# Kernel tuning notes

Measured on AMD Instinct MI355X. Metric: run time of the kernel, lower is better.

The kernel has to match this reference:

```python
import jax, jax.numpy as jnp
import numpy as np

EPSILON = 1e-05


def setup_inputs() -> dict:
    key = jax.random.key(0)
    k1, k2, k3 = jax.random.split(key, 3)
    B, T, D, K = 8, 4096, 256, 2048
    hidden_states = jax.random.normal(k1, (B, T, D), dtype=jnp.float32)
    embed_sum = jax.random.normal(k2, (K, D), dtype=jnp.float32)
    # cluster usage counts are positive in practice
    cluster_usage = jax.random.uniform(k3, (K,), dtype=jnp.float32) * 10.0 + 0.1
    return {
        "hidden_states": hidden_states,
        "embed_sum": embed_sum,
        "cluster_usage": cluster_usage,
    }


def reference(hidden_states, embed_sum, cluster_usage):
    # embed = embed_sum / clamp(cluster_usage, eps)   -> [K, D]
    embed = embed_sum / jnp.clip(cluster_usage, EPSILON, None)[:, None]

    shape = hidden_states.shape
    x = hidden_states.reshape(-1, shape[-1])  # [N, D]

    # squared L2 distances via norm expansion (argmin equals argmin of cdist p=2)
    x_sq = jnp.sum(x * x, axis=-1, keepdims=True)          # [N, 1]
    e_sq = jnp.sum(embed * embed, axis=-1)[None, :]         # [1, K]
    dots = jnp.einsum("nd,kd->nk", x, embed)               # [N, K]
    dists = x_sq - 2.0 * dots + e_sq                        # [N, K]

    embed_ind = jnp.argmin(dists, axis=-1)                 # [N]
    embed_ind = embed_ind.reshape(shape[:-1])              # [B, T]

    # decode: embedding lookup
    quantize = embed[embed_ind]                             # [B, T, D]
    return quantize, embed_ind
```

## Files before the change

### kernel.cpp

```cpp
#include <hip/hip_runtime.h>
#include <float.h>
#include <stdint.h>


#define EPSILON 1e-5f
#define DELTA   1e-3f

constexpr int D     = 256;
constexpr int K_TOT = 2048;

constexpr int RES_H      = 32768;
constexpr int ESQ_H      = 65536;
constexpr int LDS_HALVES = 69632;
constexpr int DYN_LDS    = LDS_HALVES * 2;

typedef _Float16 half8v __attribute__((ext_vector_type(8)));
typedef _Float16 half4v __attribute__((ext_vector_type(4)));
typedef float    f32x4  __attribute__((ext_vector_type(4)));

#define GLL(SRC, DST)                                                   \
  __builtin_amdgcn_global_load_lds(                                     \
      (const __attribute__((address_space(1))) void*)(SRC),             \
      (__attribute__((address_space(3))) void*)(DST), 16, 0, 0)

__global__ void prep_kernel(const float* __restrict__ es,
                            const float* __restrict__ usage,
                            _Float16* __restrict__ ec,
                            float* __restrict__ esq,
                            int* __restrict__ counter) {
  const int bx   = blockIdx.x;
  const int t    = threadIdx.x;
  const int wid  = t >> 6;
  const int lane = t & 63;
  if (bx < K_TOT / 4) {
    const int k = bx * 4 + wid;
    const float u = fmaxf(usage[k], EPSILON);
    const float4 v = *(const float4*)(es + (size_t)k * D + lane * 4);
    float4 e;
    e.x = v.x / u; e.y = v.y / u; e.z = v.z / u; e.w = v.w / u;
    half4v h, lo;
    h.x = (_Float16)e.x; lo.x = (_Float16)(e.x - (float)h.x);
    h.y = (_Float16)e.y; lo.y = (_Float16)(e.y - (float)h.y);
    h.z = (_Float16)e.z; lo.z = (_Float16)(e.z - (float)h.z);
    h.w = (_Float16)e.w; lo.w = (_Float16)(e.w - (float)h.w);
    *(half4v*)(ec + (size_t)k * 512 + lane * 4)       = h;
    *(half4v*)(ec + (size_t)k * 512 + 256 + lane * 4) = lo;
    float s = e.x * e.x + e.y * e.y + e.z * e.z + e.w * e.w;
    #pragma unroll
    for (int m = 1; m < 64; m <<= 1) s += __shfl_xor(s, m, 64);
    if (lane == 0) esq[k] = s;
  } else {
    if (t == 0) *counter = 0;
  }
}

__global__ __launch_bounds__(512, 2)
void mm_kernel(const float* __restrict__ x, const _Float16* __restrict__ ec,
               const float* __restrict__ esq, const float* __restrict__ es,
               const float* __restrict__ usage,
               float* __restrict__ out_q, float* __restrict__ out_i,
               int* __restrict__ list, int* __restrict__ counter,
               unsigned long long* __restrict__ rmin, int N) {
  extern __shared__ __align__(16) _Float16 lds[];
  const int t    = threadIdx.x;
  const int lane = t & 63;
  const int q    = lane >> 4;
  const int l15  = lane & 15;
  const int wid  = t >> 6;
  const int wn   = wid >> 1;
  const int wk   = wid & 1;
  const int n0   = blockIdx.x * 128;

  float* esq_lds = (float*)&lds[ESQ_H];
  {
    const float4 ev = *(const float4*)(esq + t * 4);
    *(float4*)&esq_lds[t * 4] = ev;
  }

  const int prow  = t >> 2;
  const int pc    = t & 3;
  const int wbase = (t >> 6) * 512 + ((t & 63) ^ ((t >> 3) & 3)) * 8;
  #pragma unroll
  for (int i = 0; i < 8; ++i) {
    const float* src = x + (size_t)(n0 + prow) * D + i * 32 + pc * 8;
    const float4 f0 = *(const float4*)src;
    const float4 f1 = *(const float4*)(src + 4);
    const float f[8] = {f0.x, f0.y, f0.z, f0.w, f1.x, f1.y, f1.z, f1.w};
    half8v hv, lv;
    #pragma unroll
    for (int e = 0; e < 8; ++e) {
      const _Float16 h = (_Float16)f[e];
      hv[e] = h;
      lv[e] = (_Float16)(f[e] - (float)h);
    }
    *(half8v*)&lds[i * 4096 + wbase]         = hv;
    *(half8v*)&lds[RES_H + i * 4096 + wbase] = lv;
  }
  __syncthreads();

  const int gA = l15 * 4 + q;
  const int sp = (gA ^ ((l15 >> 1) & 3)) * 8;

  half8v ahr[8][2];
  #pragma unroll
  for (int s = 0; s < 8; ++s)
    #pragma unroll
    for (int mi = 0; mi < 2; ++mi)
      ahr[s][mi] = *(const half8v*)&lds[s * 4096 + wn * 1024 + mi * 512 + sp];
  __syncthreads();

  const int r0 = t >> 3;
  const int cl = (t & 7) ^ (r0 & 7);
  const _Float16* pB = ec + (size_t)r0 * 512 + cl * 8;

  #pragma unroll
  for (int s = 0; s < 3; ++s) {
    const _Float16* sp0 = pB + s * 64;
    GLL(sp0,         &lds[s * 8192 + t * 8]);
    GLL(sp0 + 32768, &lds[s * 8192 + 4096 + t * 8]);
  }

  int bfoff[4][2];
  #pragma unroll
  for (int ni = 0; ni < 4; ++ni)
    #pragma unroll
    for (int j = 0; j < 2; ++j)
      bfoff[ni][j] = (wk * 64 + ni * 16 + l15) * 64 +
                     (((j << 2) + q) ^ (l15 & 7)) * 8;

  float rd0[2][4], rd1[2][4];
  int   ri0[2][4];
  #pragma unroll
  for (int mi = 0; mi < 2; ++mi)
    #pragma unroll
    for (int r = 0; r < 4; ++r) {
      rd0[mi][r] = FLT_MAX; rd1[mi][r] = FLT_MAX; ri0[mi][r] = 0x7fffffff;
    }

  for (int kt = 0; kt < 16; ++kt) {
    int   kc[4];
    float eqv[4];
    #pragma unroll
    for (int ni = 0; ni < 4; ++ni) {
      kc[ni]  = kt * 128 + wk * 64 + ni * 16 + l15;
      eqv[ni] = esq_lds[kc[ni]];
    }

    f32x4 acc[2][4] = {};

    #pragma unroll
    for (int sidx = 0; sidx < 8; ++sidx) {
      const int ss = kt * 8 + sidx;
      if (kt == 15 && sidx == 6)
        asm volatile("s_waitcnt vmcnt(2)" ::: "memory");
      else if (kt == 15 && sidx == 7)
        asm volatile("s_waitcnt vmcnt(0)" ::: "memory");
      else
        asm volatile("s_waitcnt vmcnt(4)" ::: "memory");
      __builtin_amdgcn_s_barrier();
      __builtin_amdgcn_sched_barrier(0);

      if (!(kt == 15 && sidx >= 5)) {
        const int ns = ss + 3;
        const _Float16* np = pB + (size_t)(ns >> 3) * 65536 + (ns & 7) * 64;
        const int nb = (ns & 3) * 8192;
        GLL(np,         &lds[nb + t * 8]);
        GLL(np + 32768, &lds[nb + 4096 + t * 8]);
      }

      const int bb = (ss & 3) * 8192;
      __builtin_amdgcn_s_setprio(1);
      #pragma unroll
      for (int j = 0; j < 2; ++j) {
        half8v bf[4];
        #pragma unroll
        for (int ni = 0; ni < 4; ++ni)
          bf[ni] = *(const half8v*)&lds[bb + bfoff[ni][j]];
        const int ks = (sidx & 3) * 2 + j;
        if (sidx < 4) {
          half8v al[2];
          #pragma unroll
          for (int mi = 0; mi < 2; ++mi)
            al[mi] = *(const half8v*)
                &lds[RES_H + ks * 4096 + wn * 1024 + mi * 512 + sp];
          #pragma unroll
          for (int mi = 0; mi < 2; ++mi)
            #pragma unroll
            for (int ni = 0; ni < 4; ++ni)
              acc[mi][ni] = __builtin_amdgcn_mfma_f32_16x16x32_f16(
                  ahr[ks][mi], bf[ni], acc[mi][ni], 0, 0, 0);
          #pragma unroll
          for (int mi = 0; mi < 2; ++mi)
            #pragma unroll
            for (int ni = 0; ni < 4; ++ni)
              acc[mi][ni] = __builtin_amdgcn_mfma_f32_16x16x32_f16(
                  al[mi], bf[ni], acc[mi][ni], 0, 0, 0);
        } else {
          #pragma unroll
          for (int mi = 0; mi < 2; ++mi)
            #pragma unroll
            for (int ni = 0; ni < 4; ++ni)
              acc[mi][ni] = __builtin_amdgcn_mfma_f32_16x16x32_f16(
                  ahr[ks][mi], bf[ni], acc[mi][ni], 0, 0, 0);
        }
      }
      __builtin_amdgcn_s_setprio(0);
    }

    #pragma unroll
    for (int ni = 0; ni < 4; ++ni) {
      #pragma unroll
      for (int mi = 0; mi < 2; ++mi) {
        #pragma unroll
        for (int r = 0; r < 4; ++r) {
          const float d = fmaf(-2.f, acc[mi][ni][r], eqv[ni]);
          if (d < rd0[mi][r]) {
            rd1[mi][r] = rd0[mi][r]; rd0[mi][r] = d; ri0[mi][r] = kc[ni];
          } else {
            rd1[mi][r] = fminf(rd1[mi][r], d);
          }
        }
      }
    }
  }
  __syncthreads();

  float* ex = (float*)lds;
  #pragma unroll
  for (int mi = 0; mi < 2; ++mi) {
    #pragma unroll
    for (int r = 0; r < 4; ++r) {
      float d0 = rd0[mi][r], d1 = rd1[mi][r];
      int   i0 = ri0[mi][r];
      #pragma unroll
      for (int off = 1; off < 16; off <<= 1) {
        const float od0 = __shfl_xor(d0, off, 16);
        const int   oi0 = __shfl_xor(i0, off, 16);
        const float od1 = __shfl_xor(d1, off, 16);
        if (od0 < d0 || (od0 == d0 && oi0 < i0)) {
          d1 = fminf(d0, od1); d0 = od0; i0 = oi0;
        } else {
          d1 = fminf(d1, od0);
        }
      }
      if (l15 == mi * 8 + r) {
        const int row = wn * 32 + mi * 16 + q * 4 + r;
        *(float4*)&ex[(row * 2 + wk) * 4] =
            make_float4(d0, __int_as_float(i0), d1, 0.f);
      }
    }
  }
  __syncthreads();

  {
    const int row = t >> 2;
    const int seg = t & 3;
    const float4 a = *(const float4*)&ex[(row * 2 + 0) * 4];
    const float4 b = *(const float4*)&ex[(row * 2 + 1) * 4];
    float d0, d1; int i0;
    const int ia = __float_as_int(a.y), ib = __float_as_int(b.y);
    if (b.x < a.x || (b.x == a.x && ib < ia)) {
      d0 = b.x; i0 = ib; d1 = fminf(a.x, b.z);
    } else {
      d0 = a.x; i0 = ia; d1 = fminf(a.z, b.x);
    }
    const int n = n0 + row;
    const float u  = fmaxf(usage[i0], EPSILON);
    const float4* src = (const float4*)(es + (size_t)i0 * D);
    float4*       dst = (float4*)(out_q + (size_t)n * D);
    #pragma unroll
    for (int i = 0; i < 16; ++i) {
      const int j = i * 4 + seg;
      const float4 e = src[j];
      dst[j] = make_float4(e.x / u, e.y / u, e.z / u, e.w / u);
    }
    if (seg == 0) {
      out_i[n] = (float)i0;
      if (d1 - d0 < DELTA) {
        rmin[n] = 0xFFFFFFFFFFFFFFFFull;
        const int pos = atomicAdd(counter, 1);
        list[pos] = n;
      }
    }
  }
}

__global__ void repair_kernel(const float* __restrict__ x,
                              const float* __restrict__ es,
                              const float* __restrict__ usage,
                              const float* __restrict__ esq,
                              const int* __restrict__ list,
                              const int* __restrict__ counter,
                              unsigned long long* __restrict__ rmin) {
  __shared__ float xs[256];
  const int t    = threadIdx.x;
  const int w    = t >> 6;
  const int lane = t & 63;
  const int cnt  = *counter;
  const int kseg = blockIdx.x & 7;

  for (int j = blockIdx.x >> 3; j < cnt; j += 256) {
    const int n = list[j];
    __syncthreads();
    xs[t] = x[(size_t)n * D + t];
    __syncthreads();
    const float4 xv = *(const float4*)&xs[lane * 4];

    float bd = FLT_MAX;
    int   bi = 0x7fffffff;
    const int kb0 = kseg * 256 + w * 64;
    for (int kk = 0; kk < 64; kk += 4) {
      const int kbase = kb0 + kk;
      float pd[4];
      #pragma unroll
      for (int j2 = 0; j2 < 4; ++j2) {
        const int k = kbase + j2;
        const float rs = 1.0f / fmaxf(usage[k], EPSILON);
        const float4 e = *(const float4*)(es + (size_t)k * D + lane * 4);
        float p = xv.x * (e.x * rs);
        p = fmaf(xv.y, e.y * rs, p);
        p = fmaf(xv.z, e.z * rs, p);
        pd[j2] = fmaf(xv.w, e.w * rs, p);
      }
      #pragma unroll
      for (int off = 1; off < 64; off <<= 1) {
        pd[0] += __shfl_xor(pd[0], off, 64);
        pd[1] += __shfl_xor(pd[1], off, 64);
        pd[2] += __shfl_xor(pd[2], off, 64);
        pd[3] += __shfl_xor(pd[3], off, 64);
      }
      #pragma unroll
      for (int j2 = 0; j2 < 4; ++j2) {
        const float dst = fmaf(-2.f, pd[j2], esq[kbase + j2]);
        if (dst < bd) { bd = dst; bi = kbase + j2; }
      }
    }
    if (lane == 0) {
      uint32_t ub = __float_as_uint(bd);
      ub = (ub & 0x80000000u) ? ~ub : (ub | 0x80000000u);
      const unsigned long long pk =
          ((unsigned long long)ub << 32) | (unsigned)bi;
      atomicMin(&rmin[n], pk);
    }
  }
}

__global__ void repair2_kernel(const float* __restrict__ es,
                               const float* __restrict__ usage,
                               const int* __restrict__ list,
                               const int* __restrict__ counter,
                               const unsigned long long* __restrict__ rmin,
                               float* __restrict__ out_q,
                               float* __restrict__ out_i) {
  const int t   = threadIdx.x;
  const int cnt = *counter;
  for (int j = blockIdx.x; j < cnt; j += 1024) {
    const int n   = list[j];
    const int idx = (int)(rmin[n] & 0x7fffffffu);
    const float u = fmaxf(usage[idx], EPSILON);
    out_q[(size_t)n * D + t] = es[(size_t)idx * D + t] / u;
    if (t == 0) out_i[n] = (float)idx;
  }
}

constexpr int TN = 128;
constexpr int DC = 32;
constexpr int KS = 2;
constexpr int RS = 196;

__global__ void esq_kernel(const float* __restrict__ es,
                           const float* __restrict__ usage,
                           float* __restrict__ esq) {
  const int lane = threadIdx.x & 63;
  const int w    = threadIdx.x >> 6;
  const int k    = blockIdx.x * 4 + w;
  const float u  = fmaxf(usage[k], EPSILON);
  const float4 e = *(const float4*)(es + (size_t)k * D + lane * 4);
  const float a = e.x / u, b = e.y / u, c = e.z / u, d = e.w / u;
  float s = a * a + b * b + c * c + d * d;
  #pragma unroll
  for (int m = 1; m < 64; m <<= 1) s += __shfl_xor(s, m, 64);
  if (lane == 0) esq[k] = s;
}

__global__ __launch_bounds__(256, 2)
void dist_kernel(const float* __restrict__ x,
                 const float* __restrict__ es,
                 const float* __restrict__ usage,
                 const float* __restrict__ esq,
                 float* __restrict__ bestd,
                 int* __restrict__ besti, int N) {
  __shared__ float smX[DC * RS];
  __shared__ float smE[DC * RS];
  const int t    = threadIdx.x;
  const int tx   = t & 15;
  const int ty   = t >> 4;
  const int n0   = blockIdx.x * TN;
  const int half = blockIdx.y;

  float best[8];
  int   bidx[8];
  #pragma unroll
  for (int i = 0; i < 8; ++i) { best[i] = FLT_MAX; bidx[i] = 0; }

  for (int kt = 0; kt < (K_TOT / KS) / 128; ++kt) {
    const int k0 = half * (K_TOT / KS) + kt * 128;
    float acc[8][8];
    #pragma unroll
    for (int i = 0; i < 8; ++i)
      #pragma unroll
      for (int j = 0; j < 8; ++j) acc[i][j] = 0.f;

    for (int dc = 0; dc < D; dc += DC) {
      __syncthreads();
      #pragma unroll
      for (int i = 0; i < 4; ++i) {
        const int f    = i * 256 + t;
        const int row  = f >> 3;
        const int c4   = f & 7;
        const int pcol = row + ((row >> 3) << 2);
        const float4 xv =
            *(const float4*)(x + (size_t)(n0 + row) * D + dc + c4 * 4);
        smX[(c4 * 4 + 0) * RS + pcol] = xv.x;
        smX[(c4 * 4 + 1) * RS + pcol] = xv.y;
        smX[(c4 * 4 + 2) * RS + pcol] = xv.z;
        smX[(c4 * 4 + 3) * RS + pcol] = xv.w;
        const int kk = k0 + row;
        const float rs = 1.0f / fmaxf(usage[kk], EPSILON);
        const float4 ev =
            *(const float4*)(es + (size_t)kk * D + dc + c4 * 4);
        smE[(c4 * 4 + 0) * RS + pcol] = ev.x * rs;
        smE[(c4 * 4 + 1) * RS + pcol] = ev.y * rs;
        smE[(c4 * 4 + 2) * RS + pcol] = ev.z * rs;
        smE[(c4 * 4 + 3) * RS + pcol] = ev.w * rs;
      }
      __syncthreads();
      #pragma unroll 4
      for (int d = 0; d < DC; ++d) {
        const float* px = &smX[d * RS + ty * 12];
        const float* pe = &smE[d * RS + tx * 12];
        const float4 xa = *(const float4*)px;
        const float4 xb = *(const float4*)(px + 4);
        const float4 ea = *(const float4*)pe;
        const float4 eb = *(const float4*)(pe + 4);
        const float xr[8] = {xa.x, xa.y, xa.z, xa.w, xb.x, xb.y, xb.z, xb.w};
        const float er[8] = {ea.x, ea.y, ea.z, ea.w, eb.x, eb.y, eb.z, eb.w};
        #pragma unroll
        for (int i = 0; i < 8; ++i)
          #pragma unroll
          for (int jj = 0; jj < 8; ++jj)
            acc[i][jj] = fmaf(xr[i], er[jj], acc[i][jj]);
      }
    }
    #pragma unroll
    for (int jj = 0; jj < 8; ++jj) {
      const int k = k0 + tx * 8 + jj;
      const float eq = esq[k];
      #pragma unroll
      for (int i = 0; i < 8; ++i) {
        const float dst = fmaf(-2.0f, acc[i][jj], eq);
        if (dst < best[i]) { best[i] = dst; bidx[i] = k; }
      }
    }
  }
  __syncthreads();
  float* rd = smX;
  int*   ri = (int*)smE;
  #pragma unroll
  for (int i = 0; i < 8; ++i) {
    const int r = ty * 8 + i;
    rd[tx * TN + r] = best[i];
    ri[tx * TN + r] = bidx[i];
  }
  __syncthreads();
  for (int off = 8; off >= 1; off >>= 1) {
    if (tx < off) {
      #pragma unroll
      for (int i = 0; i < 8; ++i) {
        const int r = ty * 8 + i;
        const float da = rd[tx * TN + r], db = rd[(tx + off) * TN + r];
        const int   ia = ri[tx * TN + r], ib = ri[(tx + off) * TN + r];
        if (db < da || (db == da && ib < ia)) {
          rd[tx * TN + r] = db;
          ri[tx * TN + r] = ib;
        }
      }
    }
    __syncthreads();
  }
  if (tx == 0) {
    #pragma unroll
    for (int i = 0; i < 8; ++i) {
      const int r = ty * 8 + i;
      bestd[(size_t)half * N + n0 + r] = rd[r];
      besti[(size_t)half * N + n0 + r] = ri[r];
    }
  }
}

__global__ void gather_kernel(const float* __restrict__ es,
                              const float* __restrict__ usage,
                              const float* __restrict__ bestd,
                              const int* __restrict__ besti,
                              float* __restrict__ out_q,
                              float* __restrict__ out_i, int N) {
  const int w    = threadIdx.x >> 6;
  const int lane = threadIdx.x & 63;
  const int n    = blockIdx.x * 4 + w;
  const float d0 = bestd[n];
  const float d1 = bestd[(size_t)N + n];
  const int   i0 = besti[n];
  const int   i1 = besti[(size_t)N + n];
  const int idx = (d1 < d0) ? i1 : i0;
  const float u = fmaxf(usage[idx], EPSILON);
  const float4 e = *(const float4*)(es + (size_t)idx * D + lane * 4);
  float4 qv;
  qv.x = e.x / u; qv.y = e.y / u; qv.z = e.z / u; qv.w = e.w / u;
  *(float4*)(out_q + (size_t)n * D + lane * 4) = qv;
  if (lane == 0) out_i[n] = (float)idx;
}

extern "C" void kernel_launch(void* const* d_in, const int* in_sizes, int n_in,
                              void* d_out, int out_size, void* d_ws, size_t ws_size,
                              hipStream_t stream) {
  const float* x     = (const float*)d_in[0];
  const float* es    = (const float*)d_in[1];
  const float* usage = (const float*)d_in[2];
  const int N = in_sizes[0] / D;

  float* out_q = (float*)d_out;
  float* out_i = out_q + (size_t)N * D;

  const size_t EB = (size_t)K_TOT * 512 * 2;
  const size_t off_esq  = EB;
  const size_t off_list = off_esq + 8192;
  const size_t off_cnt  = off_list + (size_t)N * 4;
  const size_t off_rmin = off_cnt + 16;
  const size_t NEED     = off_rmin + (size_t)N * 8;

  char* wsb = (char*)d_ws;

  hipError_t attr_ok = hipFuncSetAttribute(
      (const void*)mm_kernel, hipFuncAttributeMaxDynamicSharedMemorySize,
      DYN_LDS);

  if (ws_size >= NEED && attr_ok == hipSuccess && (N % 128) == 0) {
    _Float16* ec   = (_Float16*)wsb;
    float*    esq  = (float*)(wsb + off_esq);
    int*      list = (int*)(wsb + off_list);
    int*      cnt  = (int*)(wsb + off_cnt);
    unsigned long long* rmin = (unsigned long long*)(wsb + off_rmin);

    prep_kernel<<<K_TOT / 4 + 1, 256, 0, stream>>>(es, usage, ec, esq, cnt);
    mm_kernel<<<N / 128, 512, DYN_LDS, stream>>>(x, ec, esq, es, usage,
                                                 out_q, out_i, list, cnt,
                                                 rmin, N);
    repair_kernel<<<2048, 256, 0, stream>>>(x, es, usage, esq, list, cnt, rmin);
    repair2_kernel<<<1024, 256, 0, stream>>>(es, usage, list, cnt, rmin,
                                             out_q, out_i);
  } else {
    float* ws    = (float*)d_ws;
    float* esq   = ws;
    float* bestd = ws + K_TOT;
    int*   besti = (int*)(ws + K_TOT + (size_t)KS * N);
    esq_kernel<<<K_TOT / 4, 256, 0, stream>>>(es, usage, esq);
    dist_kernel<<<dim3(N / TN, KS), 256, 0, stream>>>(x, es, usage, esq,
                                                      bestd, besti, N);
    gather_kernel<<<N / 4, 256, 0, stream>>>(es, usage, bestd, besti,
                                             out_q, out_i, N);
  }
}
```

Measured before the change: 187.2 us.

## Switch distance GEMM to 32x32x16 MFMA with split hi/lo accumulators

Result: slower. 205.7 us (+9.9%).

```diff
diff --git a/kernel.cpp b/kernel.cpp
--- a/kernel.cpp
+++ b/kernel.cpp
@@ -14,9 +14,10 @@
 constexpr int LDS_HALVES = 69632;
 constexpr int DYN_LDS    = LDS_HALVES * 2;
 
-typedef _Float16 half8v __attribute__((ext_vector_type(8)));
-typedef _Float16 half4v __attribute__((ext_vector_type(4)));
-typedef float    f32x4  __attribute__((ext_vector_type(4)));
+typedef _Float16 half8v  __attribute__((ext_vector_type(8)));
+typedef _Float16 half4v  __attribute__((ext_vector_type(4)));
+typedef float    f32x4   __attribute__((ext_vector_type(4)));
+typedef float    f32x16  __attribute__((ext_vector_type(16)));
 
 #define GLL(SRC, DST)                                                   \
   __builtin_amdgcn_global_load_lds(                                     \
@@ -64,8 +65,8 @@
   extern __shared__ __align__(16) _Float16 lds[];
   const int t    = threadIdx.x;
   const int lane = t & 63;
-  const int q    = lane >> 4;
-  const int l15  = lane & 15;
+  const int l31  = lane & 31;
+  const int l5   = lane >> 5;
   const int wid  = t >> 6;
   const int wn   = wid >> 1;
   const int wk   = wid & 1;
@@ -98,15 +99,14 @@
   }
   __syncthreads();
 
-  const int gA = l15 * 4 + q;
-  const int sp = (gA ^ ((l15 >> 1) & 3)) * 8;
-
-  half8v ahr[8][2];
-  #pragma unroll
-  for (int s = 0; s < 8; ++s)
-    #pragma unroll
-    for (int mi = 0; mi < 2; ++mi)
-      ahr[s][mi] = *(const half8v*)&lds[s * 4096 + wn * 1024 + mi * 512 + sp];
+  const int ablk = (wn * 2 + ((lane >> 4) & 1)) * 512 + (lane & 15) * 32;
+  const int sw   = (lane >> 1) & 3;
+
+  half8v ahr[16];
+  #pragma unroll
+  for (int s = 0; s < 16; ++s)
+    ahr[s] = *(const half8v*)
+        &lds[(s >> 1) * 4096 + ablk + ((((s & 1) << 1) + l5) ^ sw) * 8];
   __syncthreads();
 
   const int r0 = t >> 3;
@@ -120,33 +120,24 @@
     GLL(sp0 + 32768, &lds[s * 8192 + 4096 + t * 8]);
   }
 
-  int bfoff[4][2];
-  #pragma unroll
-  for (int ni = 0; ni < 4; ++ni)
-    #pragma unroll
-    for (int j = 0; j < 2; ++j)
-      bfoff[ni][j] = (wk * 64 + ni * 16 + l15) * 64 +
-                     (((j << 2) + q) ^ (l15 & 7)) * 8;
-
-  float rd0[2][4], rd1[2][4];
-  int   ri0[2][4];
-  #pragma unroll
-  for (int mi = 0; mi < 2; ++mi)
-    #pragma unroll
-    for (int r = 0; r < 4; ++r) {
-      rd0[mi][r] = FLT_MAX; rd1[mi][r] = FLT_MAX; ri0[mi][r] = 0x7fffffff;
-    }
+  int bfoff[2][4];
+  #pragma unroll
+  for (int ni = 0; ni < 2; ++ni)
+    #pragma unroll
+    for (int ks4 = 0; ks4 < 4; ++ks4)
+      bfoff[ni][ks4] = (wk * 64 + ni * 32 + l31) * 64 +
+                       ((ks4 * 2 + l5) ^ (lane & 7)) * 8;
+
+  float rd0[16], rd1[16];
+  int   ri0[16];
+  #pragma unroll
+  for (int r = 0; r < 16; ++r) {
+    rd0[r] = FLT_MAX; rd1[r] = FLT_MAX; ri0[r] = 0x7fffffff;
+  }
 
   for (int kt = 0; kt < 16; ++kt) {
-    int   kc[4];
-    float eqv[4];
-    #pragma unroll
-    for (int ni = 0; ni < 4; ++ni) {
-      kc[ni]  = kt * 128 + wk * 64 + ni * 16 + l15;
-      eqv[ni] = esq_lds[kc[ni]];
-    }
-
-    f32x4 acc[2][4] = {};
+    f32x16 accH[2] = {};
+    f32x16 accL[2] = {};
 
     #pragma unroll
     for (int sidx = 0; sidx < 8; ++sidx) {
@@ -171,54 +162,43 @@
       const int bb = (ss & 3) * 8192;
       __builtin_amdgcn_s_setprio(1);
       #pragma unroll
-      for (int j = 0; j < 2; ++j) {
-        half8v bf[4];
-        #pragma unroll
-        for (int ni = 0; ni < 4; ++ni)
-          bf[ni] = *(const half8v*)&lds[bb + bfoff[ni][j]];
-        const int ks = (sidx & 3) * 2 + j;
+      for (int ks4 = 0; ks4 < 4; ++ks4) {
+        const int ks = (sidx & 3) * 4 + ks4;
+        const half8v b0 = *(const half8v*)&lds[bb + bfoff[0][ks4]];
+        const half8v b1 = *(const half8v*)&lds[bb + bfoff[1][ks4]];
         if (sidx < 4) {
-          half8v al[2];
-          #pragma unroll
-          for (int mi = 0; mi < 2; ++mi)
-            al[mi] = *(const half8v*)
-                &lds[RES_H + ks * 4096 + wn * 1024 + mi * 512 + sp];
-          #pragma unroll
-          for (int mi = 0; mi < 2; ++mi)
-            #pragma unroll
-            for (int ni = 0; ni < 4; ++ni)
-              acc[mi][ni] = __builtin_amdgcn_mfma_f32_16x16x32_f16(
-                  ahr[ks][mi], bf[ni], acc[mi][ni], 0, 0, 0);
-          #pragma unroll
-          for (int mi = 0; mi < 2; ++mi)
-            #pragma unroll
-            for (int ni = 0; ni < 4; ++ni)
-              acc[mi][ni] = __builtin_amdgcn_mfma_f32_16x16x32_f16(
-                  al[mi], bf[ni], acc[mi][ni], 0, 0, 0);
+          const half8v al = *(const half8v*)
+              &lds[RES_H + (ks >> 1) * 4096 + ablk +
+                   ((((ks & 1) << 1) + l5) ^ sw) * 8];
+          accH[0] = __builtin_amdgcn_mfma_f32_32x32x16_f16(ahr[ks], b0,
+                                                           accH[0], 0, 0, 0);
+          accH[1] = __builtin_amdgcn_mfma_f32_32x32x16_f16(ahr[ks], b1,
+                                                           accH[1], 0, 0, 0);
+          accL[0] = __builtin_amdgcn_mfma_f32_32x32x16_f16(al, b0,
+                                                           accL[0], 0, 0, 0);
+          accL[1] = __builtin_amdgcn_mfma_f32_32x32x16_f16(al, b1,
+                                                           accL[1], 0, 0, 0);
         } else {
-          #pragma unroll
-          for (int mi = 0; mi < 2; ++mi)
-            #pragma unroll
-            for (int ni = 0; ni < 4; ++ni)
-              acc[mi][ni] = __builtin_amdgcn_mfma_f32_16x16x32_f16(
-                  ahr[ks][mi], bf[ni], acc[mi][ni], 0, 0, 0);
+          accL[0] = __builtin_amdgcn_mfma_f32_32x32x16_f16(ahr[ks], b0,
+                                                           accL[0], 0, 0, 0);
+          accL[1] = __builtin_amdgcn_mfma_f32_32x32x16_f16(ahr[ks], b1,
+                                                           accL[1], 0, 0, 0);
         }
       }
       __builtin_amdgcn_s_setprio(0);
     }
 
     #pragma unroll
-    for (int ni = 0; ni < 4; ++ni) {
-      #pragma unroll
-      for (int mi = 0; mi < 2; ++mi) {
-        #pragma unroll
-        for (int r = 0; r < 4; ++r) {
-          const float d = fmaf(-2.f, acc[mi][ni][r], eqv[ni]);
-          if (d < rd0[mi][r]) {
-            rd1[mi][r] = rd0[mi][r]; rd0[mi][r] = d; ri0[mi][r] = kc[ni];
-          } else {
-            rd1[mi][r] = fminf(rd1[mi][r], d);
-          }
+    for (int ni = 0; ni < 2; ++ni) {
+      const int   kcol = kt * 128 + wk * 64 + ni * 32 + l31;
+      const float eqv  = esq_lds[kcol];
+      #pragma unroll
+      for (int r = 0; r < 16; ++r) {
+        const float d = fmaf(-2.f, accH[ni][r] + accL[ni][r], eqv);
+        if (d < rd0[r]) {
+          rd1[r] = rd0[r]; rd0[r] = d; ri0[r] = kcol;
+        } else {
+          rd1[r] = fminf(rd1[r], d);
         }
       }
     }
@@ -227,27 +207,24 @@
 
   float* ex = (float*)lds;
   #pragma unroll
-  for (int mi = 0; mi < 2; ++mi) {
-    #pragma unroll
-    for (int r = 0; r < 4; ++r) {
-      float d0 = rd0[mi][r], d1 = rd1[mi][r];
-      int   i0 = ri0[mi][r];
-      #pragma unroll
-      for (int off = 1; off < 16; off <<= 1) {
-        const float od0 = __shfl_xor(d0, off, 16);
-        const int   oi0 = __shfl_xor(i0, off, 16);
-        const float od1 = __shfl_xor(d1, off, 16);
-        if (od0 < d0 || (od0 == d0 && oi0 < i0)) {
-          d1 = fminf(d0, od1); d0 = od0; i0 = oi0;
-        } else {
-          d1 = fminf(d1, od0);
-        }
-      }
-      if (l15 == mi * 8 + r) {
-        const int row = wn * 32 + mi * 16 + q * 4 + r;
-        *(float4*)&ex[(row * 2 + wk) * 4] =
-            make_float4(d0, __int_as_float(i0), d1, 0.f);
-      }
+  for (int r = 0; r < 16; ++r) {
+    float d0 = rd0[r], d1 = rd1[r];
+    int   i0 = ri0[r];
+    #pragma unroll
+    for (int off = 1; off < 32; off <<= 1) {
+      const float od0 = __shfl_xor(d0, off, 32);
+      const int   oi0 = __shfl_xor(i0, off, 32);
+      const float od1 = __shfl_xor(d1, off, 32);
+      if (od0 < d0 || (od0 == d0 && oi0 < i0)) {
+        d1 = fminf(d0, od1); d0 = od0; i0 = oi0;
+      } else {
+        d1 = fminf(d1, od0);
+      }
+    }
+    if (l31 == r) {
+      const int row = wn * 32 + (r & 3) + 8 * (r >> 2) + 4 * l5;
+      *(float4*)&ex[(row * 2 + wk) * 4] =
+          make_float4(d0, __int_as_float(i0), d1, 0.f);
     }
   }
   __syncthreads();
```
